# Performance work log

Hardware: AMD Instinct MI355X
Metric: run time of the kernel (lower is better)

## Reference

```python
import jax, jax.numpy as jnp
import numpy as np

SIGMA = 1.0


def setup_inputs() -> dict:
    key = jax.random.key(0)
    z = jax.random.normal(key, (8192, 256), dtype=jnp.float32)
    return {"z": z}


def reference(z):
    n, d = z.shape
    gamma = 1.0 / (2.0 * SIGMA ** 2)
    sq = jnp.sum(z * z, axis=-1)                      # [n]
    gram = z @ z.T                                    # [n, n]
    dist_sq = sq[:, None] + sq[None, :] - 2.0 * gram  # [n, n]
    dist_sq = jnp.maximum(dist_sq, 0.0)
    term_a = jnp.mean(jnp.exp(-gamma * dist_sq))
    denom_b = 1.0 + 2.0 * gamma * SIGMA ** 2
    coeff_b = 1.0 / denom_b ** (d / 2.0)
    term_b = coeff_b * jnp.mean(jnp.exp(-(gamma / denom_b) * sq))
    term_c = 1.0 / (1.0 + 4.0 * gamma * SIGMA ** 2) ** (d / 2.0)
    return term_a - 2.0 * term_b + term_c
```

## Files before the change

kernel.cpp:

```cpp
#include <hip/hip_runtime.h>
#include <math.h>

#define N 8192
#define D 256
#define TILE 128
#define NT (N / TILE)
#define NTILES (NT * (NT + 1) / 2)
#define NPREP (N / 4)
#define LOG2E 1.4426950408889634f
#define GROUP_SZ 4096

typedef float f32x4 __attribute__((ext_vector_type(4)));
typedef int   i32x8 __attribute__((ext_vector_type(8)));

#define WS_PB_OFF 12288
#define WS_SQ_OFF 32768
#define WS_ZB_OFF 65536

__device__ __forceinline__ size_t frag_off8(int row, int k) {
    return (size_t)(row >> 4) * GROUP_SZ + ((k >> 7) << 11) + (((k >> 5) & 3) << 9)
         + ((row & 15) << 5) + (k & 31);
}

__global__ __launch_bounds__(256) void prep_kernel(const float* __restrict__ z,
                                                   unsigned char* __restrict__ zb8,
                                                   float* __restrict__ sq,
                                                   float* __restrict__ partialsB) {
    __shared__ float pb4[4];
    const int t = threadIdx.x;
    const int lane = t & 63;
    const int wave = t >> 6;
    const int row = blockIdx.x * 4 + wave;
    float4 v = ((const float4*)(z + (size_t)row * D))[lane];
    unsigned p = __builtin_amdgcn_cvt_pk_fp8_f32(v.x, v.y, 0u, false);
    p = __builtin_amdgcn_cvt_pk_fp8_f32(v.z, v.w, p, true);
    *(unsigned*)(zb8 + frag_off8(row, lane * 4)) = p;
    float s = v.x * v.x + v.y * v.y + v.z * v.z + v.w * v.w;
    #pragma unroll
    for (int off = 32; off > 0; off >>= 1) s += __shfl_xor(s, off, 64);
    if (lane == 0) {
        sq[row] = s;
        pb4[wave] = __expf(-0.25f * s);
    }
    __syncthreads();
    if (t == 0) partialsB[blockIdx.x] = pb4[0] + pb4[1] + pb4[2] + pb4[3];
}

__global__ __launch_bounds__(256) void pair_mfma_kernel(const unsigned char* __restrict__ zb8,
                                                        const float* __restrict__ sq,
                                                        float* __restrict__ partialsA) {
    __shared__ float red[4];

    int bi = 0, rem = blockIdx.x;
    while (rem >= NT - bi) { rem -= NT - bi; ++bi; }
    const int bj = bi + rem;
    const int i0 = bi * TILE, j0 = bj * TILE;

    const int t = threadIdx.x;
    const int lane = t & 63, wave = t >> 6;
    const int wi = wave >> 1, wj = wave & 1;
    const int col = lane & 15, q = lane >> 4;

    const unsigned char* pA[4];
    const unsigned char* pB[4];
    #pragma unroll
    for (int x = 0; x < 4; ++x) {
        pA[x] = zb8 + (size_t)(i0 / 16 + wi * 4 + x) * GROUP_SZ + lane * 32;
        pB[x] = zb8 + (size_t)(j0 / 16 + wj * 4 + x) * GROUP_SZ + lane * 32;
    }

    f32x4 acc[4][4];
    #pragma unroll
    for (int mt = 0; mt < 4; ++mt)
        #pragma unroll
        for (int nt = 0; nt < 4; ++nt)
            acc[mt][nt] = (f32x4){0.f, 0.f, 0.f, 0.f};

    i32x8 af0[4], bf0[4], af1[4], bf1[4];
    #pragma unroll
    for (int x = 0; x < 4; ++x) {
        af0[x] = *(const i32x8*)(pA[x]);
        bf0[x] = *(const i32x8*)(pB[x]);
    }
    #pragma unroll
    for (int x = 0; x < 4; ++x) {
        af1[x] = *(const i32x8*)(pA[x] + 2048);
        bf1[x] = *(const i32x8*)(pB[x] + 2048);
    }
    #pragma unroll
    for (int mt = 0; mt < 4; ++mt)
        #pragma unroll
        for (int nt = 0; nt < 4; ++nt)
            acc[mt][nt] = __builtin_amdgcn_mfma_scale_f32_16x16x128_f8f6f4(
                af0[mt], bf0[nt], acc[mt][nt], 0, 0, 0, 127, 0, 127);
    #pragma unroll
    for (int mt = 0; mt < 4; ++mt)
        #pragma unroll
        for (int nt = 0; nt < 4; ++nt)
            acc[mt][nt] = __builtin_amdgcn_mfma_scale_f32_16x16x128_f8f6f4(
                af1[mt], bf1[nt], acc[mt][nt], 0, 0, 0, 127, 0, 127);

    float cj[4];
    #pragma unroll
    for (int nt = 0; nt < 4; ++nt)
        cj[nt] = -0.5f * LOG2E * sq[j0 + wj * 64 + nt * 16 + col];

    float local = 0.f;
    if (bi != bj) {
        #pragma unroll
        for (int mt = 0; mt < 4; ++mt)
            #pragma unroll
            for (int r = 0; r < 4; ++r) {
                const float ci = -0.5f * LOG2E * sq[i0 + wi * 64 + mt * 16 + q * 4 + r];
                #pragma unroll
                for (int nt = 0; nt < 4; ++nt)
                    local += exp2f(fmaf(acc[mt][nt][r], LOG2E, ci) + cj[nt]);
            }
        local *= 2.f;
    } else {
        #pragma unroll
        for (int mt = 0; mt < 4; ++mt)
            #pragma unroll
            for (int r = 0; r < 4; ++r) {
                const int li = wi * 64 + mt * 16 + q * 4 + r;
                const float ci = -0.5f * LOG2E * sq[i0 + li];
                #pragma unroll
                for (int nt = 0; nt < 4; ++nt) {
                    const int lj = wj * 64 + nt * 16 + col;
                    float arg = fminf(fmaf(acc[mt][nt][r], LOG2E, ci) + cj[nt], 0.f);
                    local += (li == lj) ? 1.0f : exp2f(arg);
                }
            }
    }

    #pragma unroll
    for (int off = 32; off > 0; off >>= 1) local += __shfl_xor(local, off, 64);
    if (lane == 0) red[wave] = local;
    __syncthreads();
    if (t == 0) partialsA[blockIdx.x] = red[0] + red[1] + red[2] + red[3];
}

__global__ __launch_bounds__(256) void final_kernel(const float* __restrict__ partialsA,
                                                    const float* __restrict__ partialsB,
                                                    float* __restrict__ out) {
    __shared__ double redA[4], redB[4];
    const int t = threadIdx.x;
    double sa = 0.0, sb = 0.0;
    for (int i = t; i < NTILES; i += 256) sa += (double)partialsA[i];
    for (int i = t; i < NPREP; i += 256) sb += (double)partialsB[i];
    #pragma unroll
    for (int off = 32; off > 0; off >>= 1) {
        sa += __shfl_xor(sa, off, 64);
        sb += __shfl_xor(sb, off, 64);
    }
    if ((t & 63) == 0) { redA[t >> 6] = sa; redB[t >> 6] = sb; }
    __syncthreads();
    if (t == 0) {
        double A = redA[0] + redA[1] + redA[2] + redA[3];
        double B = redB[0] + redB[1] + redB[2] + redB[3];
        double term_a = A / ((double)N * (double)N);
        double coeff_b = ldexp(1.0, -128);
        double term_c = 1.0;
        for (int i = 0; i < 128; ++i) term_c /= 3.0;
        out[0] = (float)(term_a - 2.0 * coeff_b * (B / (double)N) + term_c);
    }
}

extern "C" void kernel_launch(void* const* d_in, const int* in_sizes, int n_in,
                              void* d_out, int out_size, void* d_ws, size_t ws_size,
                              hipStream_t stream) {
    const float* z = (const float*)d_in[0];
    float* partialsA = (float*)d_ws;
    float* partialsB = (float*)((char*)d_ws + WS_PB_OFF);
    float* sq = (float*)((char*)d_ws + WS_SQ_OFF);
    unsigned char* zb8 = (unsigned char*)((char*)d_ws + WS_ZB_OFF);
    float* out = (float*)d_out;

    hipLaunchKernelGGL(prep_kernel, dim3(NPREP), dim3(256), 0, stream, z, zb8, sq, partialsB);
    hipLaunchKernelGGL(pair_mfma_kernel, dim3(NTILES), dim3(256), 0, stream, zb8, sq, partialsA);
    hipLaunchKernelGGL(final_kernel, dim3(1), dim3(256), 0, stream, partialsA, partialsB, out);
}
```

Baseline: 92.36 us.

## Stage FP8 operand tiles through LDS via direct global-to-LDS loads

Changes the FP8 fragment layout so each 32-byte operand fragment is split into two 16-byte halves, then has the whole block copy its A and B tiles into 64KB of shared memory with global_load_lds. Waves then read their MFMA fragments from LDS, so each wave no longer issues its own redundant global loads of the same tiles. The cost is 64KB of LDS per block, which limits occupancy, plus an added barrier. The reduction scratch now reuses the A buffer.

```diff
diff --git a/kernel.cpp b/kernel.cpp
--- a/kernel.cpp
+++ b/kernel.cpp
@@ -10,7 +10,11 @@
 #define LOG2E 1.4426950408889634f
 #define GROUP_SZ 4096
 
+#define GLOBAL_AS __attribute__((address_space(1)))
+#define LDS_AS    __attribute__((address_space(3)))
+
 typedef float f32x4 __attribute__((ext_vector_type(4)));
+typedef int   i32x4 __attribute__((ext_vector_type(4)));
 typedef int   i32x8 __attribute__((ext_vector_type(8)));
 
 #define WS_PB_OFF 12288
@@ -18,8 +22,10 @@
 #define WS_ZB_OFF 65536
 
 __device__ __forceinline__ size_t frag_off8(int row, int k) {
-    return (size_t)(row >> 4) * GROUP_SZ + ((k >> 7) << 11) + (((k >> 5) & 3) << 9)
-         + ((row & 15) << 5) + (k & 31);
+    const int g = row >> 4, m = row & 15;
+    const int ks = (k >> 7) & 1, q = (k >> 5) & 3, j = k & 31;
+    return (size_t)g * GROUP_SZ + ks * 2048 + ((j & 16) << 6)
+         + (q << 8) + (m << 4) + (j & 15);
 }
 
 __global__ __launch_bounds__(256) void prep_kernel(const float* __restrict__ z,
@@ -49,7 +55,8 @@
 __global__ __launch_bounds__(256) void pair_mfma_kernel(const unsigned char* __restrict__ zb8,
                                                         const float* __restrict__ sq,
                                                         float* __restrict__ partialsA) {
-    __shared__ float red[4];
+    __shared__ __align__(16) unsigned char As[32768];
+    __shared__ __align__(16) unsigned char Bs[32768];
 
     int bi = 0, rem = blockIdx.x;
     while (rem >= NT - bi) { rem -= NT - bi; ++bi; }
@@ -61,13 +68,17 @@
     const int wi = wave >> 1, wj = wave & 1;
     const int col = lane & 15, q = lane >> 4;
 
-    const unsigned char* pA[4];
-    const unsigned char* pB[4];
+    const unsigned char* srcA = zb8 + (size_t)(i0 >> 4) * GROUP_SZ;
+    const unsigned char* srcB = zb8 + (size_t)(j0 >> 4) * GROUP_SZ;
     #pragma unroll
-    for (int x = 0; x < 4; ++x) {
-        pA[x] = zb8 + (size_t)(i0 / 16 + wi * 4 + x) * GROUP_SZ + lane * 32;
-        pB[x] = zb8 + (size_t)(j0 / 16 + wj * 4 + x) * GROUP_SZ + lane * 32;
+    for (int i = 0; i < 8; ++i) {
+        const int off = (i * 256 + t) * 16;
+        __builtin_amdgcn_global_load_lds((const GLOBAL_AS unsigned int*)(srcA + off),
+                                         (LDS_AS unsigned int*)(As + off), 16, 0, 0);
+        __builtin_amdgcn_global_load_lds((const GLOBAL_AS unsigned int*)(srcB + off),
+                                         (LDS_AS unsigned int*)(Bs + off), 16, 0, 0);
     }
+    __syncthreads();
 
     f32x4 acc[4][4];
     #pragma unroll
@@ -76,29 +87,27 @@
         for (int nt = 0; nt < 4; ++nt)
             acc[mt][nt] = (f32x4){0.f, 0.f, 0.f, 0.f};
 
-    i32x8 af0[4], bf0[4], af1[4], bf1[4];
     #pragma unroll
-    for (int x = 0; x < 4; ++x) {
-        af0[x] = *(const i32x8*)(pA[x]);
-        bf0[x] = *(const i32x8*)(pB[x]);
+    for (int ks = 0; ks < 2; ++ks) {
+        i32x8 af[4], bf[4];
+        #pragma unroll
+        for (int x = 0; x < 4; ++x) {
+            const unsigned char* a = As + (wi * 4 + x) * GROUP_SZ + ks * 2048 + lane * 16;
+            i32x4 lo = *(const i32x4*)a;
+            i32x4 hi = *(const i32x4*)(a + 1024);
+            af[x] = __builtin_shufflevector(lo, hi, 0, 1, 2, 3, 4, 5, 6, 7);
+            const unsigned char* b = Bs + (wj * 4 + x) * GROUP_SZ + ks * 2048 + lane * 16;
+            i32x4 blo = *(const i32x4*)b;
+            i32x4 bhi = *(const i32x4*)(b + 1024);
+            bf[x] = __builtin_shufflevector(blo, bhi, 0, 1, 2, 3, 4, 5, 6, 7);
+        }
+        #pragma unroll
+        for (int mt = 0; mt < 4; ++mt)
+            #pragma unroll
+            for (int nt = 0; nt < 4; ++nt)
+                acc[mt][nt] = __builtin_amdgcn_mfma_scale_f32_16x16x128_f8f6f4(
+                    af[mt], bf[nt], acc[mt][nt], 0, 0, 0, 127, 0, 127);
     }
-    #pragma unroll
-    for (int x = 0; x < 4; ++x) {
-        af1[x] = *(const i32x8*)(pA[x] + 2048);
-        bf1[x] = *(const i32x8*)(pB[x] + 2048);
-    }
-    #pragma unroll
-    for (int mt = 0; mt < 4; ++mt)
-        #pragma unroll
-        for (int nt = 0; nt < 4; ++nt)
-            acc[mt][nt] = __builtin_amdgcn_mfma_scale_f32_16x16x128_f8f6f4(
-                af0[mt], bf0[nt], acc[mt][nt], 0, 0, 0, 127, 0, 127);
-    #pragma unroll
-    for (int mt = 0; mt < 4; ++mt)
-        #pragma unroll
-        for (int nt = 0; nt < 4; ++nt)
-            acc[mt][nt] = __builtin_amdgcn_mfma_scale_f32_16x16x128_f8f6f4(
-                af1[mt], bf1[nt], acc[mt][nt], 0, 0, 0, 127, 0, 127);
 
     float cj[4];
     #pragma unroll
@@ -135,6 +144,8 @@
 
     #pragma unroll
     for (int off = 32; off > 0; off >>= 1) local += __shfl_xor(local, off, 64);
+    __syncthreads();
+    float* red = (float*)As;
     if (lane == 0) red[wave] = local;
     __syncthreads();
     if (t == 0) partialsA[blockIdx.x] = red[0] + red[1] + red[2] + red[3];
```

New measurement: 90.18 us. -2.4%, faster.
